# Optimization experiments

Hardware: AMD Instinct MI355X
Metric: run time of the kernel (lower is better)

The kernel has to match this reference:

```python
import jax, jax.numpy as jnp
import numpy as np

B, T, D = 2, 4096, 768
H = 12
HD = D // H  # 64
SCALE = 1.0 / np.sqrt(HD)


def setup_inputs() -> dict:
    key = jax.random.key(0)
    k1, k2, k3 = jax.random.split(key, 3)
    x = jax.random.normal(k1, (B, T, D), dtype=jnp.float32)
    W_qkv = jax.random.normal(k2, (D, 3 * D), dtype=jnp.float32) * (1.0 / np.sqrt(D))
    b_qkv = jnp.zeros((3 * D,), dtype=jnp.float32)
    W_out = jax.random.normal(k3, (D, D), dtype=jnp.float32) * (1.0 / np.sqrt(D))
    b_out = jnp.zeros((D,), dtype=jnp.float32)
    return {"x": x, "W_qkv": W_qkv, "b_qkv": b_qkv, "W_out": W_out, "b_out": b_out}


def reference(x, W_qkv, b_qkv, W_out, b_out):
    Bx, Tx, C = x.shape
    qkv = x @ W_qkv + b_qkv                                  # [B,T,3D]
    qkv = qkv.reshape(Bx, Tx, 3, H, HD).transpose(2, 0, 3, 1, 4)  # [3,B,H,T,hd]
    q, k, v = qkv[0], qkv[1], qkv[2]
    scores = jnp.einsum('bhqd,bhkd->bhqk', q, k) * SCALE      # [B,H,T,T]
    causal = jnp.tril(jnp.ones((Tx, Tx), dtype=bool))
    scores = jnp.where(causal[None, None], scores, -jnp.inf)
    attn = jax.nn.softmax(scores, axis=-1)
    out = jnp.einsum('bhqk,bhkd->bhqd', attn, v)              # [B,H,T,hd]
    out = out.transpose(0, 2, 1, 3).reshape(Bx, Tx, C)        # [B,T,D]
    return out @ W_out + b_out
```

## Files before the change

kernel.cpp:

```cpp
#include <hip/hip_runtime.h>
#include <cstdint>
#include <cstddef>

typedef _Float16 f16x8 __attribute__((ext_vector_type(8)));
typedef _Float16 f16x4 __attribute__((ext_vector_type(4)));
typedef float    f32x4 __attribute__((ext_vector_type(4)));

#define AS_GLOBAL __attribute__((address_space(1)))
#define AS_LDS    __attribute__((address_space(3)))

__device__ __forceinline__ void load16_to_lds(const _Float16* g, _Float16* l) {
    __builtin_amdgcn_global_load_lds((const AS_GLOBAL void*)g, (AS_LDS void*)l, 16, 0, 0);
}

#define BB   2
#define TT   4096
#define DD   768
#define NH   12
#define HDIM 64
#define D3   2304
#define SC2  (0.125f * 1.44269504088896f)

__global__ __launch_bounds__(256) void prep(const float* __restrict__ x,
                                            _Float16* __restrict__ Xh,
                                            const float* __restrict__ Wqkv,
                                            _Float16* __restrict__ Wqkvt,
                                            const float* __restrict__ Wout,
                                            _Float16* __restrict__ Wot) {
    const int bid = blockIdx.x, tid = threadIdx.x;
    if (bid < 6144) {
        const int i = bid * 1024 + tid * 4;
        float4 v = *(const float4*)(x + i);
        f16x4 h;
        h[0] = (_Float16)v.x; h[1] = (_Float16)v.y;
        h[2] = (_Float16)v.z; h[3] = (_Float16)v.w;
        *(f16x4*)(Xh + i) = h;
        return;
    }
    __shared__ float tile[32][33];
    const float* in; _Float16* out; int C, bx, by;
    if (bid < 7872) {
        const int t = bid - 6144;
        in = Wqkv; out = Wqkvt; C = 2304;
        bx = (t % 72) * 32; by = (t / 72) * 32;
    } else {
        const int t = bid - 7872;
        in = Wout; out = Wot; C = 768;
        bx = (t % 24) * 32; by = (t / 24) * 32;
    }
    const int R = 768;
    const int tx = tid & 31, ty = tid >> 5;
#pragma unroll
    for (int j = 0; j < 32; j += 8)
        tile[ty + j][tx] = in[(size_t)(by + ty + j) * C + bx + tx];
    __syncthreads();
#pragma unroll
    for (int j = 0; j < 32; j += 8)
        out[(size_t)(bx + ty + j) * R + by + tx] = (_Float16)tile[tx][ty + j];
}

template <typename OutT, int IM, int IN>
__device__ __forceinline__ void gemm_body(const _Float16* __restrict__ A,
                                          const _Float16* __restrict__ Bt,
                                          const float* __restrict__ bias, bool bias_row,
                                          OutT* __restrict__ C, int N, int K,
                                          int m0, int n0,
                                          _Float16* As, _Float16* Bs) {
    const int tid  = threadIdx.x;
    const int wave = tid >> 6, lane = tid & 63, quad = lane >> 4, l16 = lane & 15;
    const int wm = (wave & 1) * (IM * 16), wn = (wave >> 1) * (IN * 16);
    constexpr int RA = 2 * IM * 16;
    constexpr int RB = 2 * IN * 16;
    constexpr int PA = RA / 64;
    constexpr int PB = RB / 64;

    f32x4 acc[IM][IN];
#pragma unroll
    for (int i = 0; i < IM; ++i)
#pragma unroll
        for (int n = 0; n < IN; ++n) acc[i][n] = f32x4{0.f, 0.f, 0.f, 0.f};

    auto stage = [&](int buf, int k0) {
#pragma unroll
        for (int p = 0; p < PA; ++p) {
            const int j = p * 256 + wave * 64 + lane;
            const int row = j >> 2, part = j & 3;
            load16_to_lds(A + (size_t)(m0 + row) * K + k0 + part * 8,
                          As + buf * (RA * 32) + (p * 256 + wave * 64) * 8);
        }
#pragma unroll
        for (int p = 0; p < PB; ++p) {
            const int j = p * 256 + wave * 64 + lane;
            const int row = j >> 2, part = j & 3;
            load16_to_lds(Bt + (size_t)(n0 + row) * K + k0 + part * 8,
                          Bs + buf * (RB * 32) + (p * 256 + wave * 64) * 8);
        }
    };

    const int nt = K >> 5;
    stage(0, 0);
    int cur = 0;
    for (int t = 0; t < nt; ++t) {
        __syncthreads();
        if (t + 1 < nt) stage(cur ^ 1, (t + 1) * 32);
#pragma unroll
        for (int i = 0; i < IM; ++i) {
            f16x8 a = *(const f16x8*)(As + cur * (RA * 32) + (wm + i * 16 + l16) * 32 + quad * 8);
#pragma unroll
            for (int n = 0; n < IN; ++n) {
                f16x8 b = *(const f16x8*)(Bs + cur * (RB * 32) + (wn + n * 16 + l16) * 32 + quad * 8);
                acc[i][n] = __builtin_amdgcn_mfma_f32_16x16x32_f16(a, b, acc[i][n], 0, 0, 0);
            }
        }
        cur ^= 1;
    }
#pragma unroll
    for (int i = 0; i < IM; ++i)
#pragma unroll
        for (int n = 0; n < IN; ++n)
#pragma unroll
            for (int r = 0; r < 4; ++r) {
                const int row = m0 + wm + i * 16 + quad * 4 + r;
                const int col = n0 + wn + n * 16 + l16;
                const float bv = bias_row ? bias[row] : bias[col];
                C[(size_t)row * N + col] = (OutT)(acc[i][n][r] + bv);
            }
}

__global__ __launch_bounds__(256, 3) void gemm_qkv(const _Float16* __restrict__ Xh,
                                                   const _Float16* __restrict__ Wqkvt,
                                                   const float* __restrict__ bqkv,
                                                   _Float16* __restrict__ QKh,
                                                   _Float16* __restrict__ VtG) {
    __shared__ __align__(16) _Float16 As[2 * 192 * 32];
    __shared__ __align__(16) _Float16 Bs[2 * 192 * 32];
    const int bid = blockIdx.x;
    if (bid < 512) {
        const int xcd = bid & 7, j = bid >> 3;
        const int by = xcd + 8 * (j >> 3);
        const int bx = j & 7;
        gemm_body<_Float16, 4, 6>(Xh, Wqkvt, bqkv, false, QKh, 1536, DD,
                                  by * 128, bx * 192, As, Bs);
    } else {
        const int t = bid - 512;
        const int xcd = t & 7, j = t >> 3;
        const int bn = xcd + 8 * (j >> 2);
        const int bm = j & 3;
        gemm_body<_Float16, 6, 4>(Wqkvt + (size_t)1536 * DD, Xh, bqkv + 1536, true, VtG,
                                  8192, DD, bm * 192, bn * 128, As, Bs);
    }
}

__global__ __launch_bounds__(256) void gemm_out(const _Float16* __restrict__ A,
                                                const _Float16* __restrict__ Bt,
                                                const float* __restrict__ bias,
                                                float* __restrict__ C) {
    __shared__ __align__(16) _Float16 As[2 * 64 * 32];
    __shared__ __align__(16) _Float16 Bs[2 * 128 * 32];
    const int L = blockIdx.x;
    const int xcd = L & 7, j = L >> 3;
    const int by = xcd + 8 * (j / 6);
    const int bx = j % 6;
    gemm_body<float, 2, 4>(A, Bt, bias, false, C, DD, DD,
                           by * 64, bx * 128, As, Bs);
}

__global__ __launch_bounds__(256, 5) void attn_kernel(const _Float16* __restrict__ qk,
                                                      const _Float16* __restrict__ vt,
                                                      _Float16* __restrict__ ao) {
    __shared__ __align__(16) _Float16 Ks[2][64 * 64];
    __shared__ __align__(16) _Float16 Vs[2][64 * 64];

    const int L    = blockIdx.x;
    const int xcd  = L & 7;
    const int r_   = L >> 3;
    const int gIdx = r_ % 3;
    const int qt   = 63 - r_ / 3;
    const int g    = gIdx * 8 + xcd;
    const int b = g / NH, h = g % NH;

    const int tid = threadIdx.x;
    const int wave = tid >> 6, lane = tid & 63, quad = lane >> 4, l16 = lane & 15;
    const int wq = wave >> 1, wk = wave & 1;

    f16x4 ones4;
#pragma unroll
    for (int j = 0; j < 4; ++j) ones4[j] = (_Float16)1.0f;

    int vK[2], vV[2];
#pragma unroll
    for (int p = 0; p < 2; ++p) {
        const int j   = wave * 16 + p * 8 + (lane >> 3);
        const int cdk = (lane & 7) ^ (j & 7);
        const int cdv = (lane & 7) ^ (((j & 3) << 1) | ((j >> 2) & 1));
        vK[p] = (b * TT + j) * 1536 + DD + h * HDIM + cdk * 8;
        vV[p] = (h * HDIM + j) * 8192 + b * TT + cdv * 8;
    }
    auto stage = [&](int buf, int k0) {
        const int kK = k0 * 1536;
#pragma unroll
        for (int p = 0; p < 2; ++p) {
            load16_to_lds(qk + (vK[p] + kK), Ks[buf] + (wave * 16 + p * 8) * 64);
            load16_to_lds(vt + (vV[p] + k0), Vs[buf] + (wave * 16 + p * 8) * 64);
        }
    };

    const int q0 = qt * 64;
    const int nkt = qt + 1;
    const int qrow0 = q0 + wq * 32;
    const int qr_lane = qrow0 + l16;
    const int rv = ((l16 & 3) << 1) | ((l16 >> 2) & 1);
    f16x8 aq[2][2];
#pragma unroll
    for (int mq = 0; mq < 2; ++mq) {
        const int qoff = (b * TT + qrow0 + mq * 16 + l16) * 1536 + h * HDIM + quad * 8;
        const _Float16 sc = (_Float16)SC2;
        aq[mq][0] = *(const f16x8*)(qk + qoff) * sc;
        aq[mq][1] = *(const f16x8*)(qk + qoff + 32) * sc;
    }
    f32x4 o[2][4], lac[2];
#pragma unroll
    for (int mq = 0; mq < 2; ++mq) {
#pragma unroll
        for (int n = 0; n < 4; ++n) o[mq][n] = f32x4{0.f, 0.f, 0.f, 0.f};
        lac[mq] = f32x4{0.f, 0.f, 0.f, 0.f};
    }

    stage(0, 0);
    int cur = 0;
    for (int kt = 0; kt < nkt; ++kt) {
        __syncthreads();
        if (kt + 1 < nkt) stage(cur ^ 1, (kt + 1) * 64);

        f32x4 s[2][2];
        f16x4 pa[2][2];
#pragma unroll
        for (int mq = 0; mq < 2; ++mq)
#pragma unroll
            for (int n1 = 0; n1 < 2; ++n1) s[mq][n1] = f32x4{0.f, 0.f, 0.f, 0.f};

        auto qk_half = [&](int n1) {
#pragma unroll
            for (int kh = 0; kh < 2; ++kh) {
                const int rowK = (wk * 2 + n1) * 16 + l16;
                const int pos = (kh * 4 + quad) ^ (l16 & 7);
                f16x8 bk = *(const f16x8*)(Ks[cur] + rowK * 64 + pos * 8);
                s[0][n1] = __builtin_amdgcn_mfma_f32_16x16x32_f16(bk, aq[0][kh], s[0][n1], 0, 0, 0);
                s[1][n1] = __builtin_amdgcn_mfma_f32_16x16x32_f16(bk, aq[1][kh], s[1][n1], 0, 0, 0);
            }
        };
        auto mask_half = [&](int n1) {
#pragma unroll
            for (int mq = 0; mq < 2; ++mq) {
                const int qr = qr_lane + mq * 16;
                const int kg0 = kt * 64 + wk * 32 + n1 * 16 + quad * 4;
#pragma unroll
                for (int r = 0; r < 4; ++r)
                    if (kg0 + r > qr) s[mq][n1][r] = -1e30f;
            }
        };
        auto exp_half = [&](int n1) {
#pragma unroll
            for (int mq = 0; mq < 2; ++mq)
#pragma unroll
                for (int r = 0; r < 4; ++r)
                    pa[mq][n1][r] = (_Float16)__builtin_amdgcn_exp2f(s[mq][n1][r]);
        };
        auto pv_half = [&](int n1) {
            f16x4 ap0 = pa[0][n1], ap1 = pa[1][n1];
            lac[0] = __builtin_amdgcn_mfma_f32_16x16x16f16(ap0, ones4, lac[0], 0, 0, 0);
            lac[1] = __builtin_amdgcn_mfma_f32_16x16x16f16(ap1, ones4, lac[1], 0, 0, 0);
#pragma unroll
            for (int n = 0; n < 4; ++n) {
                const int rowV = n * 16 + l16;
                const int lc  = wk * 4 + n1 * 2 + (quad >> 1);
                const int pc  = lc ^ rv;
                f16x4 bv = *(const f16x4*)(Vs[cur] + rowV * 64 + pc * 8 + (quad & 1) * 4);
                o[0][n] = __builtin_amdgcn_mfma_f32_16x16x16f16(ap0, bv, o[0][n], 0, 0, 0);
                o[1][n] = __builtin_amdgcn_mfma_f32_16x16x16f16(ap1, bv, o[1][n], 0, 0, 0);
            }
        };

        const bool last = (kt == nkt - 1);
        __builtin_amdgcn_s_setprio(1);
        qk_half(0);
        __builtin_amdgcn_s_setprio(0);
        if (last) mask_half(0);
        exp_half(0);
        __builtin_amdgcn_s_setprio(1);
        qk_half(1);
        pv_half(0);
        __builtin_amdgcn_s_setprio(0);
        if (last) mask_half(1);
        exp_half(1);
        __builtin_amdgcn_s_setprio(1);
        pv_half(1);
        __builtin_amdgcn_s_setprio(0);
        cur ^= 1;
    }

    __syncthreads();
    float* const Ksf = (float*)&Ks[0][0];
    float* const Vsf = (float*)&Vs[0][0];
    if (wk) {
#pragma unroll
        for (int mq = 0; mq < 2; ++mq) {
            if (l16 == 0)
                *(f32x4*)(Vsf + wq * 32 + mq * 16 + quad * 4) = lac[mq];
#pragma unroll
            for (int n = 0; n < 4; ++n)
                *(f32x4*)(Ksf + wq * 2048 + (mq * 4 + n) * 256 + lane * 4) = o[mq][n];
        }
    }
    __syncthreads();
    if (!wk) {
#pragma unroll
        for (int mq = 0; mq < 2; ++mq) {
            f32x4 lp = *(const f32x4*)(Vsf + wq * 32 + mq * 16 + quad * 4);
            f32x4 inv;
#pragma unroll
            for (int r = 0; r < 4; ++r) inv[r] = 1.0f / (lac[mq][r] + lp[r]);
#pragma unroll
            for (int n = 0; n < 4; ++n) {
                f32x4 op = *(const f32x4*)(Ksf + wq * 2048 + (mq * 4 + n) * 256 + lane * 4);
#pragma unroll
                for (int r = 0; r < 4; ++r) {
                    const int ooff = (b * TT + qrow0 + mq * 16 + quad * 4 + r) * DD + h * HDIM + l16;
                    ao[ooff + n * 16] = (_Float16)((o[mq][n][r] + op[r]) * inv[r]);
                }
            }
        }
    }
}

extern "C" void kernel_launch(void* const* d_in, const int* in_sizes, int n_in,
                              void* d_out, int out_size, void* d_ws, size_t ws_size,
                              hipStream_t stream) {
    const float* x     = (const float*)d_in[0];
    const float* Wqkv  = (const float*)d_in[1];
    const float* bqkv  = (const float*)d_in[2];
    const float* Wout  = (const float*)d_in[3];
    const float* bout  = (const float*)d_in[4];
    float* out = (float*)d_out;

    char* ws = (char*)d_ws;
    _Float16* Xh    = (_Float16*)ws;  ws += (size_t)BB * TT * DD * 2;
    _Float16* Wqkvt = (_Float16*)ws;  ws += (size_t)D3 * DD * 2;
    _Float16* Wot   = (_Float16*)ws;  ws += (size_t)DD * DD * 2;
    _Float16* QKh   = (_Float16*)ws;  ws += (size_t)BB * TT * 1536 * 2;
    _Float16* VtG   = (_Float16*)ws;  ws += (size_t)DD * BB * TT * 2;
    _Float16* AOh   = (_Float16*)ws;  ws += (size_t)BB * TT * DD * 2;

    prep<<<8448, 256, 0, stream>>>(x, Xh, Wqkv, Wqkvt, Wout, Wot);

    gemm_qkv<<<768, 256, 0, stream>>>(Xh, Wqkvt, bqkv, QKh, VtG);

    attn_kernel<<<1536, 256, 0, stream>>>(QKh, VtG, AOh);

    gemm_out<<<768, 256, 0, stream>>>(AOh, Wot, bout, out);
}
```

Measured before the change: 221.3 us.

## Use 16x16x32 MFMA for PV by permuting K rows in LDS staging

Permutes the K-tile row order when staging into LDS so that each lane's QK score outputs line up as eight consecutive key positions. Both score halves can then be packed into one f16x8 operand and fed to 16x16x32 MFMAs for the PV product and the row-sum accumulation. This halves the number of PV MFMA instructions and replaces 4-element V loads with 8-element ones, using a simpler shared XOR swizzle for K and V. In exchange, the PV work no longer overlaps the second QK/exp half and instead runs at the end of each tile, which reduces instruction interleaving.

```diff
diff --git a/kernel.cpp b/kernel.cpp
--- a/kernel.cpp
+++ b/kernel.cpp
@@ -183,18 +183,18 @@
     const int wave = tid >> 6, lane = tid & 63, quad = lane >> 4, l16 = lane & 15;
     const int wq = wave >> 1, wk = wave & 1;
 
-    f16x4 ones4;
-#pragma unroll
-    for (int j = 0; j < 4; ++j) ones4[j] = (_Float16)1.0f;
+    f16x8 ones8;
+#pragma unroll
+    for (int j = 0; j < 8; ++j) ones8[j] = (_Float16)1.0f;
 
     int vK[2], vV[2];
 #pragma unroll
     for (int p = 0; p < 2; ++p) {
         const int j   = wave * 16 + p * 8 + (lane >> 3);
-        const int cdk = (lane & 7) ^ (j & 7);
-        const int cdv = (lane & 7) ^ (((j & 3) << 1) | ((j >> 2) & 1));
-        vK[p] = (b * TT + j) * 1536 + DD + h * HDIM + cdk * 8;
-        vV[p] = (h * HDIM + j) * 8192 + b * TT + cdv * 8;
+        const int sig = (j & ~12) | ((j & 8) >> 1) | ((j & 4) << 1);
+        const int cd  = (lane & 7) ^ (j & 7);
+        vK[p] = (b * TT + sig) * 1536 + DD + h * HDIM + cd * 8;
+        vV[p] = (h * HDIM + j) * 8192 + b * TT + cd * 8;
     }
     auto stage = [&](int buf, int k0) {
         const int kK = k0 * 1536;
@@ -209,7 +209,7 @@
     const int nkt = qt + 1;
     const int qrow0 = q0 + wq * 32;
     const int qr_lane = qrow0 + l16;
-    const int rv = ((l16 & 3) << 1) | ((l16 >> 2) & 1);
+    const int rowKbase = wk * 32 + 16 * (l16 >> 3) + 4 * ((l16 >> 2) & 1) + (l16 & 3);
     f16x8 aq[2][2];
 #pragma unroll
     for (int mq = 0; mq < 2; ++mq) {
@@ -233,7 +233,7 @@
         if (kt + 1 < nkt) stage(cur ^ 1, (kt + 1) * 64);
 
         f32x4 s[2][2];
-        f16x4 pa[2][2];
+        f16x8 pa8[2];
 #pragma unroll
         for (int mq = 0; mq < 2; ++mq)
 #pragma unroll
@@ -242,7 +242,7 @@
         auto qk_half = [&](int n1) {
 #pragma unroll
             for (int kh = 0; kh < 2; ++kh) {
-                const int rowK = (wk * 2 + n1) * 16 + l16;
+                const int rowK = rowKbase + 8 * n1;
                 const int pos = (kh * 4 + quad) ^ (l16 & 7);
                 f16x8 bk = *(const f16x8*)(Ks[cur] + rowK * 64 + pos * 8);
                 s[0][n1] = __builtin_amdgcn_mfma_f32_16x16x32_f16(bk, aq[0][kh], s[0][n1], 0, 0, 0);
@@ -253,7 +253,7 @@
 #pragma unroll
             for (int mq = 0; mq < 2; ++mq) {
                 const int qr = qr_lane + mq * 16;
-                const int kg0 = kt * 64 + wk * 32 + n1 * 16 + quad * 4;
+                const int kg0 = kt * 64 + wk * 32 + 8 * quad + 4 * n1;
 #pragma unroll
                 for (int r = 0; r < 4; ++r)
                     if (kg0 + r > qr) s[mq][n1][r] = -1e30f;
@@ -264,21 +264,7 @@
             for (int mq = 0; mq < 2; ++mq)
 #pragma unroll
                 for (int r = 0; r < 4; ++r)
-                    pa[mq][n1][r] = (_Float16)__builtin_amdgcn_exp2f(s[mq][n1][r]);
-        };
-        auto pv_half = [&](int n1) {
-            f16x4 ap0 = pa[0][n1], ap1 = pa[1][n1];
-            lac[0] = __builtin_amdgcn_mfma_f32_16x16x16f16(ap0, ones4, lac[0], 0, 0, 0);
-            lac[1] = __builtin_amdgcn_mfma_f32_16x16x16f16(ap1, ones4, lac[1], 0, 0, 0);
-#pragma unroll
-            for (int n = 0; n < 4; ++n) {
-                const int rowV = n * 16 + l16;
-                const int lc  = wk * 4 + n1 * 2 + (quad >> 1);
-                const int pc  = lc ^ rv;
-                f16x4 bv = *(const f16x4*)(Vs[cur] + rowV * 64 + pc * 8 + (quad & 1) * 4);
-                o[0][n] = __builtin_amdgcn_mfma_f32_16x16x16f16(ap0, bv, o[0][n], 0, 0, 0);
-                o[1][n] = __builtin_amdgcn_mfma_f32_16x16x16f16(ap1, bv, o[1][n], 0, 0, 0);
-            }
+                    pa8[mq][n1 * 4 + r] = (_Float16)__builtin_amdgcn_exp2f(s[mq][n1][r]);
         };
 
         const bool last = (kt == nkt - 1);
@@ -289,12 +275,21 @@
         exp_half(0);
         __builtin_amdgcn_s_setprio(1);
         qk_half(1);
-        pv_half(0);
         __builtin_amdgcn_s_setprio(0);
         if (last) mask_half(1);
         exp_half(1);
+
         __builtin_amdgcn_s_setprio(1);
-        pv_half(1);
+        lac[0] = __builtin_amdgcn_mfma_f32_16x16x32_f16(pa8[0], ones8, lac[0], 0, 0, 0);
+        lac[1] = __builtin_amdgcn_mfma_f32_16x16x32_f16(pa8[1], ones8, lac[1], 0, 0, 0);
+#pragma unroll
+        for (int n = 0; n < 4; ++n) {
+            const int rowV = n * 16 + l16;
+            const int pc = (wk * 4 + quad) ^ (l16 & 7);
+            f16x8 bv = *(const f16x8*)(Vs[cur] + rowV * 64 + pc * 8);
+            o[0][n] = __builtin_amdgcn_mfma_f32_16x16x32_f16(pa8[0], bv, o[0][n], 0, 0, 0);
+            o[1][n] = __builtin_amdgcn_mfma_f32_16x16x32_f16(pa8[1], bv, o[1][n], 0, 0, 0);
+        }
         __builtin_amdgcn_s_setprio(0);
         cur ^= 1;
     }
```

Measured after the change: 214.0 us. 3.3% less time.
